# Kernel tuning notes

Hardware: AMD Instinct MI355X
Metric: run time of the kernel (lower is better)

## Reference

```python
import jax, jax.numpy as jnp
import numpy as np

NUM_EXPERTS = 16
TOP_K = 8
INIT_STD = 0.02

def setup_inputs() -> dict:
    key = jax.random.key(0)
    ks = jax.random.split(key, 5)
    B, S, H, I, E = 2, 2048, 2048, 768, NUM_EXPERTS
    return {
        "hidden_states": jax.random.normal(ks[0], (B, S, H), jnp.float32),
        "w_router": jax.random.normal(ks[1], (H, E), jnp.float32) * INIT_STD,
        "w_gate": jax.random.normal(ks[2], (E, H, I), jnp.float32) * INIT_STD,
        "w_up": jax.random.normal(ks[3], (E, H, I), jnp.float32) * INIT_STD,
        "w_down": jax.random.normal(ks[4], (E, I, H), jnp.float32) * INIT_STD,
    }

def reference(hidden_states, w_router, w_gate, w_up, w_down):
    # Router: logits -> fp32 softmax -> top-k -> renormalize (norm_topk_prob=True)
    router_logits = jnp.einsum("bsh,he->bse", hidden_states, w_router)  # [B,S,E]
    routing_weights = jax.nn.softmax(router_logits.astype(jnp.float32), axis=-1)
    topk_w, topk_idx = jax.lax.top_k(routing_weights, k=TOP_K)  # [B,S,K]
    topk_w = topk_w / topk_w.sum(axis=-1, keepdims=True)
    # Dense per-expert combine weights [B,S,E] (sum over top-k slots matching each expert)
    dense_w = jnp.sum(jax.nn.one_hot(topk_idx, NUM_EXPERTS, dtype=topk_w.dtype) * topk_w[..., None], axis=2)
    dense_w = dense_w.astype(hidden_states.dtype)
    # Every expert runs on all tokens (as in the source loop), vectorized over E
    gate = jax.nn.silu(jnp.einsum("bsh,ehi->besi", hidden_states, w_gate))  # [B,E,S,I]
    up = jnp.einsum("bsh,ehi->besi", hidden_states, w_up)
    expert_out = jnp.einsum("besi,eih->besh", gate * up, w_down)  # [B,E,S,H]
    final = jnp.einsum("bse,besh->bsh", dense_w, expert_out)
    return final, router_logits
```

## Files before the change

### kernel.cpp

```cpp
#include <hip/hip_runtime.h>
#include <hip/hip_bf16.h>


typedef __attribute__((ext_vector_type(8))) short short8;
typedef __attribute__((ext_vector_type(4))) float f32x4;

#define NUM_T 4096
#define DH    2048
#define DI    768
#define NE    16
#define DKD   (NE*DI)
#define MAXMT 20
#define FINAL_ELEMS ((size_t)NUM_T*DH)


static __device__ __forceinline__ unsigned short f2bf(float f) {
  unsigned int u = __builtin_bit_cast(unsigned int, f);
  u += 0x7fffu + ((u >> 16) & 1u);
  return (unsigned short)(u >> 16);
}

static __device__ __forceinline__ float bf2f(unsigned short b) {
  unsigned int u = ((unsigned int)b) << 16;
  return __builtin_bit_cast(float, u);
}

static __device__ __forceinline__ void gload16(const void* g, void* l) {
  __builtin_amdgcn_global_load_lds(
      (__attribute__((address_space(1))) void*)(g),
      (__attribute__((address_space(3))) void*)(l), 16, 0, 0);
}


__global__ __launch_bounds__(256)
void cvt_hidden_k(const float* __restrict__ in, unsigned short* __restrict__ out) {
  size_t i = (size_t)blockIdx.x * 256 + threadIdx.x;
  const float4* p = (const float4*)in + i * 2;
  float4 a = p[0], b = p[1];
  short8 v;
  v[0] = (short)f2bf(a.x); v[1] = (short)f2bf(a.y);
  v[2] = (short)f2bf(a.z); v[3] = (short)f2bf(a.w);
  v[4] = (short)f2bf(b.x); v[5] = (short)f2bf(b.y);
  v[6] = (short)f2bf(b.z); v[7] = (short)f2bf(b.w);
  *(short8*)(out + i * 8) = v;
}


__global__ __launch_bounds__(256)
void transpose_cvt_k(const float* __restrict__ in, unsigned short* __restrict__ out,
                     int R, int C, long inStrideE, long outStrideE, int outLD) {
  __shared__ float tile[32][33];
  const float* inE = in + (size_t)blockIdx.z * inStrideE;
  unsigned short* outE = out + (size_t)blockIdx.z * outStrideE;
  int c0 = blockIdx.x * 32, r0 = blockIdx.y * 32;
  int tx = threadIdx.x, ty = threadIdx.y;
#pragma unroll
  for (int i = 0; i < 4; i++)
    tile[ty * 4 + i][tx] = inE[(size_t)(r0 + ty * 4 + i) * C + c0 + tx];
  __syncthreads();
#pragma unroll
  for (int i = 0; i < 4; i++) {
    int c = ty * 4 + i;
    outE[(size_t)(c0 + c) * outLD + r0 + tx] = f2bf(tile[tx][c]);
  }
}


__global__ __launch_bounds__(256)
void router_k(const float* __restrict__ x, const float* __restrict__ wr,
              float* __restrict__ logits_out, unsigned short* __restrict__ dwb) {
  int t = blockIdx.x;
  int tid = threadIdx.x, lane = tid & 63, wid = tid >> 6;
  float acc[16];
#pragma unroll
  for (int e = 0; e < 16; e++) acc[e] = 0.f;
  const float* xt = x + (size_t)t * DH;
  for (int i = tid; i < DH; i += 256) {
    float hv = xt[i];
    const float4* w4 = (const float4*)(wr + (size_t)i * 16);
#pragma unroll
    for (int q = 0; q < 4; q++) {
      float4 w = w4[q];
      acc[q * 4 + 0] += hv * w.x; acc[q * 4 + 1] += hv * w.y;
      acc[q * 4 + 2] += hv * w.z; acc[q * 4 + 3] += hv * w.w;
    }
  }
#pragma unroll
  for (int e = 0; e < 16; e++) {
#pragma unroll
    for (int off = 32; off; off >>= 1) acc[e] += __shfl_xor(acc[e], off, 64);
  }
  __shared__ float red[4][16];
  if (lane == 0) {
#pragma unroll
    for (int e = 0; e < 16; e++) red[wid][e] = acc[e];
  }
  __syncthreads();
  if (tid == 0) {
    float lg[16];
#pragma unroll
    for (int e = 0; e < 16; e++) lg[e] = red[0][e] + red[1][e] + red[2][e] + red[3][e];
    float mx = lg[0];
#pragma unroll
    for (int e = 1; e < 16; e++) mx = fmaxf(mx, lg[e]);
    float p[16], s = 0.f;
#pragma unroll
    for (int e = 0; e < 16; e++) { p[e] = __expf(lg[e] - mx); s += p[e]; }
    float inv = 1.f / s;
#pragma unroll
    for (int e = 0; e < 16; e++) p[e] *= inv;
    float tmp[16];
#pragma unroll
    for (int e = 0; e < 16; e++) tmp[e] = p[e];
    int idx[8]; float val[8]; float ts = 0.f;
#pragma unroll
    for (int k = 0; k < 8; k++) {
      int b = 0; float bv = tmp[0];
#pragma unroll
      for (int e = 1; e < 16; e++) { if (tmp[e] > bv) { bv = tmp[e]; b = e; } }
      idx[k] = b; val[k] = bv; tmp[b] = -1.f; ts += bv;
    }
    float dw[16];
#pragma unroll
    for (int e = 0; e < 16; e++) dw[e] = 0.f;
    float invt = 1.f / ts;
#pragma unroll
    for (int k = 0; k < 8; k++) dw[idx[k]] += val[k] * invt;
#pragma unroll
    for (int e = 0; e < 16; e++) {
      dwb[(size_t)t * 16 + e] = f2bf(dw[e]);
      logits_out[(size_t)t * 16 + e] = lg[e];
    }
  }
}


__global__ __launch_bounds__(256)
void build_lists_k(const unsigned short* __restrict__ dwb,
                   unsigned short* __restrict__ lst) {
  int e = blockIdx.x;
  int tid = threadIdx.x;
  unsigned short loc[16]; int c = 0;
#pragma unroll
  for (int j = 0; j < 16; j++) {
    int t = tid * 16 + j;
    if (dwb[(size_t)t * 16 + e] != 0) loc[c++] = (unsigned short)t;
  }
  __shared__ int sc[256];
  __shared__ int pre[257];
  sc[tid] = c;
  __syncthreads();
  if (tid == 0) {
    int s = 0;
    for (int i = 0; i < 256; i++) { pre[i] = s; s += sc[i]; }
    pre[256] = s;
  }
  __syncthreads();
  unsigned short* L = lst + (size_t)e * NUM_T;
  int base = pre[tid];
  for (int j = 0; j < c; j++) L[base + j] = loc[j];
  int total = pre[256];
  for (int i = total + tid; i < NUM_T; i += 256) L[i] = 0xFFFFu;
}


__global__ __launch_bounds__(256)
void zfill_k(short8* __restrict__ p) {
  size_t i = (size_t)blockIdx.x * 256 + threadIdx.x;
  short8 z = {0,0,0,0,0,0,0,0};
  p[i] = z;
}


__global__ __launch_bounds__(256, 3)
void gateup_k(const unsigned short* __restrict__ hbf,
              const unsigned short* __restrict__ wgbt,
              const unsigned short* __restrict__ wubt,
              const unsigned short* __restrict__ dwb,
              const unsigned short* __restrict__ lst,
              unsigned short* __restrict__ hs) {
  const int bxr = blockIdx.x;
  const int wl  = (bxr & 7) * 480 + (bxr >> 3);
  const int e   = wl / 240;
  const int rem = wl - e * 240;
  const int n0  = (rem / MAXMT) * 64;
  const int m0  = (rem % MAXMT) * 128;

  const unsigned short* L = lst + (size_t)e * NUM_T;
  if (L[m0] == 0xFFFFu) return;

  const int tid = threadIdx.x, lane = tid & 63, wid = tid >> 6;
  const int wm = wid >> 1, wn = wid & 1;
  const int lr = lane & 15, lgp = lane >> 4;

  __shared__ alignas(16) unsigned short As [3 * 128 * 32];
  __shared__ alignas(16) unsigned short Bgs[3 *  64 * 32];
  __shared__ alignas(16) unsigned short Bus[3 *  64 * 32];

  f32x4 zero = {0.f, 0.f, 0.f, 0.f};
  f32x4 accg[4][2], accu[4][2];
#pragma unroll
  for (int m = 0; m < 4; m++)
#pragma unroll
    for (int n = 0; n < 2; n++) { accg[m][n] = zero; accu[m][n] = zero; }

  const unsigned short* wgE = wgbt + (size_t)e * DI * DH;
  const unsigned short* wuE = wubt + (size_t)e * DI * DH;

  const int srow    = lane >> 2;
  const int schunk8 = (((lane & 3) - ((lane >> 3) & 3)) & 3) * 8;

  const int ar0 = m0 + wid * 32 + srow, ar1 = ar0 + 16;
  const unsigned short t0 = L[ar0], t1 = L[ar1];
  const size_t prow0 = (t0 == 0xFFFFu) ? 0 : (size_t)t0;
  const size_t prow1 = (t1 == 0xFFFFu) ? 0 : (size_t)t1;
  const size_t brow = (size_t)(n0 + wid * 16 + srow);

  const int slot8 = (((lane >> 4) + ((lane >> 1) & 3)) & 3) * 8;

  auto stage = [&](int b, int k0) {
    unsigned short* Ab = As  + b * 4096 + wid * 1024;
    unsigned short* Gb = Bgs + b * 2048 + wid * 512;
    unsigned short* Ub = Bus + b * 2048 + wid * 512;
    gload16(hbf + prow0 * DH + k0 + schunk8, Ab);
    gload16(hbf + prow1 * DH + k0 + schunk8, Ab + 512);
    gload16(wgE + brow  * DH + k0 + schunk8, Gb);
    gload16(wuE + brow  * DH + k0 + schunk8, Ub);
  };

  auto compute = [&](int b) {
    const unsigned short* Ab = As  + b * 4096;
    const unsigned short* Gb = Bgs + b * 2048;
    const unsigned short* Ub = Bus + b * 2048;
    short8 a[4], bg[2], bu[2];
#pragma unroll
    for (int m = 0; m < 4; m++)
      a[m] = *(const short8*)(Ab + (wm * 64 + m * 16 + lr) * 32 + slot8);
#pragma unroll
    for (int n = 0; n < 2; n++) {
      bg[n] = *(const short8*)(Gb + (wn * 32 + n * 16 + lr) * 32 + slot8);
      bu[n] = *(const short8*)(Ub + (wn * 32 + n * 16 + lr) * 32 + slot8);
    }
#pragma unroll
    for (int m = 0; m < 4; m++)
#pragma unroll
      for (int n = 0; n < 2; n++) {
        accg[m][n] = __builtin_amdgcn_mfma_f32_16x16x32_bf16(a[m], bg[n], accg[m][n], 0, 0, 0);
        accu[m][n] = __builtin_amdgcn_mfma_f32_16x16x32_bf16(a[m], bu[n], accu[m][n], 0, 0, 0);
      }
  };

  const int NT = DH / 32;
  stage(0, 0);
  stage(1, 32);
  int bc = 0, bs = 2;
#pragma unroll 1
  for (int i = 0; i < NT - 1; ++i) {
    asm volatile("s_waitcnt vmcnt(4)" ::: "memory");
    __builtin_amdgcn_s_barrier();
    __builtin_amdgcn_sched_barrier(0);
    compute(bc);
    if (i + 2 < NT) stage(bs, (i + 2) * 32);
    bc = (bc == 2) ? 0 : bc + 1;
    bs = (bs == 2) ? 0 : bs + 1;
  }
  asm volatile("s_waitcnt vmcnt(0)" ::: "memory");
  __builtin_amdgcn_s_barrier();
  __builtin_amdgcn_sched_barrier(0);
  compute(bc);

#pragma unroll
  for (int m = 0; m < 4; m++) {
#pragma unroll
    for (int r = 0; r < 4; r++) {
      int mrow = m0 + wm * 64 + m * 16 + 4 * lgp + r;
      unsigned short tp = L[mrow];
      if (tp == 0xFFFFu) continue;
      float w = bf2f(dwb[(size_t)tp * 16 + e]);
#pragma unroll
      for (int n = 0; n < 2; n++) {
        float g = accg[m][n][r], u = accu[m][n][r];
        float sig = 1.f / (1.f + __expf(-g));
        float val = g * sig * u * w;
        hs[(size_t)tp * DKD + e * DI + n0 + wn * 32 + n * 16 + lr] = f2bf(val);
      }
    }
  }
}


__global__ __launch_bounds__(256, 3)
void down_k(const unsigned short* __restrict__ hsb,
            const unsigned short* __restrict__ wdbt,
            float* __restrict__ outp) {
  const int bxr = blockIdx.x;
  const int w   = (bxr & 7) * 64 + (bxr >> 3);
  const int m0  = (w & 31) << 7;
  const int n0  = (w >> 5) << 7;

  const int tid = threadIdx.x, lane = tid & 63, wid = tid >> 6;
  const int wm = wid >> 1, wn = wid & 1;
  const int lr = lane & 15, lgp = lane >> 4;

  __shared__ alignas(16) unsigned short As[3 * 128 * 32];
  __shared__ alignas(16) unsigned short Bs[3 * 128 * 32];

  f32x4 zero = {0.f, 0.f, 0.f, 0.f};
  f32x4 acc[4][4];
#pragma unroll
  for (int m = 0; m < 4; m++)
#pragma unroll
    for (int n = 0; n < 4; n++) acc[m][n] = zero;

  const int srow    = lane >> 2;
  const int schunk8 = (((lane & 3) - ((lane >> 3) & 3)) & 3) * 8;
  const int sOff0   = wid * 1024;
  const int sOff1   = sOff0 + 512;
  const size_t arow0 = (size_t)(m0 + wid * 32 + srow), arow1 = arow0 + 16;
  const size_t brow0 = (size_t)(n0 + wid * 32 + srow), brow1 = brow0 + 16;
  const int slot8 = (((lane >> 4) + ((lane >> 1) & 3)) & 3) * 8;

  auto stage = [&](int b, int k0) {
    unsigned short* Ab = As + b * 4096;
    unsigned short* Bb = Bs + b * 4096;
    gload16(hsb  + arow0 * DKD + k0 + schunk8, Ab + sOff0);
    gload16(hsb  + arow1 * DKD + k0 + schunk8, Ab + sOff1);
    gload16(wdbt + brow0 * DKD + k0 + schunk8, Bb + sOff0);
    gload16(wdbt + brow1 * DKD + k0 + schunk8, Bb + sOff1);
  };

  auto compute = [&](int bsel) {
    const unsigned short* Ab = As + bsel * 4096;
    const unsigned short* Bb = Bs + bsel * 4096;
    short8 a[4], b[4];
#pragma unroll
    for (int m = 0; m < 4; m++)
      a[m] = *(const short8*)(Ab + (size_t)(wm * 64 + m * 16 + lr) * 32 + slot8);
#pragma unroll
    for (int n = 0; n < 4; n++)
      b[n] = *(const short8*)(Bb + (size_t)(wn * 64 + n * 16 + lr) * 32 + slot8);
#pragma unroll
    for (int m = 0; m < 4; m++)
#pragma unroll
      for (int n = 0; n < 4; n++)
        acc[m][n] = __builtin_amdgcn_mfma_f32_16x16x32_bf16(a[m], b[n], acc[m][n], 0, 0, 0);
  };

  const int NT = DKD / 32;
  stage(0, 0);
  stage(1, 32);
  int bc = 0, bs = 2;
#pragma unroll 1
  for (int i = 0; i < NT - 1; ++i) {
    asm volatile("s_waitcnt vmcnt(4)" ::: "memory");
    __builtin_amdgcn_s_barrier();
    __builtin_amdgcn_sched_barrier(0);
    compute(bc);
    if (i + 2 < NT) stage(bs, (i + 2) * 32);
    bc = (bc == 2) ? 0 : bc + 1;
    bs = (bs == 2) ? 0 : bs + 1;
  }
  asm volatile("s_waitcnt vmcnt(0)" ::: "memory");
  __builtin_amdgcn_s_barrier();
  __builtin_amdgcn_sched_barrier(0);
  compute(bc);

#pragma unroll
  for (int m = 0; m < 4; m++)
#pragma unroll
    for (int r = 0; r < 4; r++) {
      int t = m0 + wm * 64 + m * 16 + 4 * lgp + r;
#pragma unroll
      for (int n = 0; n < 4; n++)
        outp[(size_t)t * DH + n0 + wn * 64 + n * 16 + lr] = acc[m][n][r];
    }
}


extern "C" void kernel_launch(void* const* d_in, const int* in_sizes, int n_in,
                              void* d_out, int out_size, void* d_ws, size_t ws_size,
                              hipStream_t stream) {
  const float* x  = (const float*)d_in[0];
  const float* wr = (const float*)d_in[1];
  const float* wg = (const float*)d_in[2];
  const float* wu = (const float*)d_in[3];
  const float* wd = (const float*)d_in[4];

  float* outF = (float*)d_out;
  float* outL = outF + FINAL_ELEMS;

  if (ws_size < 218365952ull) return;
  char* ws = (char*)d_ws;
  unsigned short* hbf  = (unsigned short*)(ws);
  unsigned short* wgbt = (unsigned short*)(ws + 16777216);
  unsigned short* wubt = (unsigned short*)(ws + 67108864);
  unsigned short* hs   = (unsigned short*)(ws + 117440512);
  unsigned short* dwb  = (unsigned short*)(ws + 218103808);
  unsigned short* lst  = (unsigned short*)(ws + 218234880);
  unsigned short* wdbt = wgbt;

  cvt_hidden_k<<<4096, 256, 0, stream>>>(x, hbf);
  transpose_cvt_k<<<dim3(24, 64, 16), dim3(32, 8), 0, stream>>>(
      wg, wgbt, 2048, 768, (long)2048 * 768, (long)768 * 2048, 2048);
  transpose_cvt_k<<<dim3(24, 64, 16), dim3(32, 8), 0, stream>>>(
      wu, wubt, 2048, 768, (long)2048 * 768, (long)768 * 2048, 2048);
  router_k<<<4096, 256, 0, stream>>>(x, wr, outL, dwb);
  build_lists_k<<<16, 256, 0, stream>>>(dwb, lst);
  zfill_k<<<24576, 256, 0, stream>>>((short8*)hs);
  gateup_k<<<3840, 256, 0, stream>>>(hbf, wgbt, wubt, dwb, lst, hs);
  transpose_cvt_k<<<dim3(64, 24, 16), dim3(32, 8), 0, stream>>>(
      wd, wdbt, 768, 2048, (long)768 * 2048, 768L, 12288);
  down_k<<<512, 256, 0, stream>>>(hs, wdbt, outF);
}
```

Baseline: 729.0 us.

## Compact per-expert activations and run grouped down projection with slot reduction

The gate/up output is now stored compacted per expert, so only routed token rows exist, instead of as a dense token-by-(expert*I) matrix that needed zero-filling. The down projection becomes a grouped GEMM per expert over only those routed rows, with K=768 instead of 12288. It writes bf16 partial outputs into per-top-k-slot buffers, which a separate kernel sums into the final fp32 output. The work is split into two token halves to fit the workspace. This removes the zero fill and the dense down GEMM's wasted FLOPs, at the cost of extra bf16 partial traffic, a reduction pass, and bf16 rounding of the partials before summation.

```diff
diff --git a/kernel.cpp b/kernel.cpp
--- a/kernel.cpp
+++ b/kernel.cpp
@@ -11,6 +11,8 @@
 #define NE    16
 #define DKD   (NE*DI)
 #define MAXMT 20
+#define HSC_CAP 2560
+#define TOK_HALF 2048
 #define FINAL_ELEMS ((size_t)NUM_T*DH)
 
 
@@ -68,7 +70,8 @@
 
 __global__ __launch_bounds__(256)
 void router_k(const float* __restrict__ x, const float* __restrict__ wr,
-              float* __restrict__ logits_out, unsigned short* __restrict__ dwb) {
+              float* __restrict__ logits_out, unsigned short* __restrict__ dwb,
+              unsigned char* __restrict__ slt) {
   int t = blockIdx.x;
   int tid = threadIdx.x, lane = tid & 63, wid = tid >> 6;
   float acc[16];
@@ -121,14 +124,16 @@
       idx[k] = b; val[k] = bv; tmp[b] = -1.f; ts += bv;
     }
     float dw[16];
-#pragma unroll
-    for (int e = 0; e < 16; e++) dw[e] = 0.f;
+    unsigned char sl[16];
+#pragma unroll
+    for (int e = 0; e < 16; e++) { dw[e] = 0.f; sl[e] = 0xFF; }
     float invt = 1.f / ts;
 #pragma unroll
-    for (int k = 0; k < 8; k++) dw[idx[k]] += val[k] * invt;
+    for (int k = 0; k < 8; k++) { dw[idx[k]] += val[k] * invt; sl[idx[k]] = (unsigned char)k; }
 #pragma unroll
     for (int e = 0; e < 16; e++) {
       dwb[(size_t)t * 16 + e] = f2bf(dw[e]);
+      slt[(size_t)t * 16 + e] = sl[e];
       logits_out[(size_t)t * 16 + e] = lg[e];
     }
   }
@@ -137,14 +142,18 @@
 
 __global__ __launch_bounds__(256)
 void build_lists_k(const unsigned short* __restrict__ dwb,
-                   unsigned short* __restrict__ lst) {
+                   const unsigned char* __restrict__ slt,
+                   unsigned short* __restrict__ lst, int* __restrict__ meta) {
   int e = blockIdx.x;
   int tid = threadIdx.x;
   unsigned short loc[16]; int c = 0;
 #pragma unroll
   for (int j = 0; j < 16; j++) {
     int t = tid * 16 + j;
-    if (dwb[(size_t)t * 16 + e] != 0) loc[c++] = (unsigned short)t;
+    if (dwb[(size_t)t * 16 + e] != 0) {
+      unsigned short s = slt[(size_t)t * 16 + e];
+      loc[c++] = (unsigned short)(t | (s << 12));
+    }
   }
   __shared__ int sc[256];
   __shared__ int pre[257];
@@ -161,14 +170,7 @@
   for (int j = 0; j < c; j++) L[base + j] = loc[j];
   int total = pre[256];
   for (int i = total + tid; i < NUM_T; i += 256) L[i] = 0xFFFFu;
-}
-
-
-__global__ __launch_bounds__(256)
-void zfill_k(short8* __restrict__ p) {
-  size_t i = (size_t)blockIdx.x * 256 + threadIdx.x;
-  short8 z = {0,0,0,0,0,0,0,0};
-  p[i] = z;
+  if (tid == 0) { meta[e * 2] = pre[128]; meta[e * 2 + 1] = total; }
 }
 
 
@@ -178,7 +180,7 @@
               const unsigned short* __restrict__ wubt,
               const unsigned short* __restrict__ dwb,
               const unsigned short* __restrict__ lst,
-              unsigned short* __restrict__ hs) {
+              unsigned short* __restrict__ hsC) {
   const int bxr = blockIdx.x;
   const int wl  = (bxr & 7) * 480 + (bxr >> 3);
   const int e   = wl / 240;
@@ -187,7 +189,7 @@
   const int m0  = (rem % MAXMT) * 128;
 
   const unsigned short* L = lst + (size_t)e * NUM_T;
-  if (L[m0] == 0xFFFFu) return;
+  if (L[m0] & 0x8000) return;
 
   const int tid = threadIdx.x, lane = tid & 63, wid = tid >> 6;
   const int wm = wid >> 1, wn = wid & 1;
@@ -212,8 +214,8 @@
 
   const int ar0 = m0 + wid * 32 + srow, ar1 = ar0 + 16;
   const unsigned short t0 = L[ar0], t1 = L[ar1];
-  const size_t prow0 = (t0 == 0xFFFFu) ? 0 : (size_t)t0;
-  const size_t prow1 = (t1 == 0xFFFFu) ? 0 : (size_t)t1;
+  const size_t prow0 = (t0 & 0x8000) ? 0 : (size_t)(t0 & 0xFFF);
+  const size_t prow1 = (t1 & 0x8000) ? 0 : (size_t)(t1 & 0xFFF);
   const size_t brow = (size_t)(n0 + wid * 16 + srow);
 
   const int slot8 = (((lane >> 4) + ((lane >> 1) & 3)) & 3) * 8;
@@ -274,15 +276,16 @@
 #pragma unroll
     for (int r = 0; r < 4; r++) {
       int mrow = m0 + wm * 64 + m * 16 + 4 * lgp + r;
-      unsigned short tp = L[mrow];
-      if (tp == 0xFFFFu) continue;
+      unsigned short en = L[mrow];
+      if (en & 0x8000) continue;
+      int tp = en & 0xFFF;
       float w = bf2f(dwb[(size_t)tp * 16 + e]);
 #pragma unroll
       for (int n = 0; n < 2; n++) {
         float g = accg[m][n][r], u = accu[m][n][r];
         float sig = 1.f / (1.f + __expf(-g));
         float val = g * sig * u * w;
-        hs[(size_t)tp * DKD + e * DI + n0 + wn * 32 + n * 16 + lr] = f2bf(val);
+        hsC[((size_t)e * HSC_CAP + mrow) * DI + n0 + wn * 32 + n * 16 + lr] = f2bf(val);
       }
     }
   }
@@ -290,13 +293,22 @@
 
 
 __global__ __launch_bounds__(256, 3)
-void down_k(const unsigned short* __restrict__ hsb,
-            const unsigned short* __restrict__ wdbt,
-            float* __restrict__ outp) {
+void down_half_k(const unsigned short* __restrict__ hsC,
+                 const unsigned short* __restrict__ wdbt,
+                 const unsigned short* __restrict__ lst,
+                 const int* __restrict__ meta,
+                 unsigned short* __restrict__ slotbuf, int hf) {
   const int bxr = blockIdx.x;
-  const int w   = (bxr & 7) * 64 + (bxr >> 3);
-  const int m0  = (w & 31) << 7;
-  const int n0  = (w >> 5) << 7;
+  const int wl  = (bxr & 7) * 320 + (bxr >> 3);
+  const int e   = wl / 160;
+  const int rem = wl - e * 160;
+  const int n0  = (rem / 10) * 128;
+  const int m0  = (rem % 10) * 128;
+
+  const int rs = hf ? meta[e * 2] : 0;
+  const int re = hf ? meta[e * 2 + 1] : meta[e * 2];
+  const int rcount = re - rs;
+  if (m0 >= rcount) return;
 
   const int tid = threadIdx.x, lane = tid & 63, wid = tid >> 6;
   const int wm = wid >> 1, wn = wid & 1;
@@ -316,17 +328,20 @@
   const int schunk8 = (((lane & 3) - ((lane >> 3) & 3)) & 3) * 8;
   const int sOff0   = wid * 1024;
   const int sOff1   = sOff0 + 512;
-  const size_t arow0 = (size_t)(m0 + wid * 32 + srow), arow1 = arow0 + 16;
+  const size_t arow0 = (size_t)(e * HSC_CAP + rs + m0 + wid * 32 + srow);
+  const size_t arow1 = arow0 + 16;
   const size_t brow0 = (size_t)(n0 + wid * 32 + srow), brow1 = brow0 + 16;
   const int slot8 = (((lane >> 4) + ((lane >> 1) & 3)) & 3) * 8;
+
+  const unsigned short* wdE = wdbt + (size_t)e * DI;
 
   auto stage = [&](int b, int k0) {
     unsigned short* Ab = As + b * 4096;
     unsigned short* Bb = Bs + b * 4096;
-    gload16(hsb  + arow0 * DKD + k0 + schunk8, Ab + sOff0);
-    gload16(hsb  + arow1 * DKD + k0 + schunk8, Ab + sOff1);
-    gload16(wdbt + brow0 * DKD + k0 + schunk8, Bb + sOff0);
-    gload16(wdbt + brow1 * DKD + k0 + schunk8, Bb + sOff1);
+    gload16(hsC + arow0 * DI + k0 + schunk8, Ab + sOff0);
+    gload16(hsC + arow1 * DI + k0 + schunk8, Ab + sOff1);
+    gload16(wdE + brow0 * DKD + k0 + schunk8, Bb + sOff0);
+    gload16(wdE + brow1 * DKD + k0 + schunk8, Bb + sOff1);
   };
 
   auto compute = [&](int bsel) {
@@ -346,7 +361,7 @@
         acc[m][n] = __builtin_amdgcn_mfma_f32_16x16x32_bf16(a[m], b[n], acc[m][n], 0, 0, 0);
   };
 
-  const int NT = DKD / 32;
+  const int NT = DI / 32;
   stage(0, 0);
   stage(1, 32);
   int bc = 0, bs = 2;
@@ -365,15 +380,46 @@
   __builtin_amdgcn_sched_barrier(0);
   compute(bc);
 
-#pragma unroll
-  for (int m = 0; m < 4; m++)
+  const unsigned short* L = lst + (size_t)e * NUM_T;
+#pragma unroll
+  for (int m = 0; m < 4; m++) {
 #pragma unroll
     for (int r = 0; r < 4; r++) {
-      int t = m0 + wm * 64 + m * 16 + 4 * lgp + r;
+      int gr = m0 + wm * 64 + m * 16 + 4 * lgp + r;
+      if (gr >= rcount) continue;
+      unsigned short en = L[rs + gr];
+      int t  = en & 0xFFF;
+      int s  = (en >> 12) & 7;
+      int tl = t - hf * TOK_HALF;
 #pragma unroll
       for (int n = 0; n < 4; n++)
-        outp[(size_t)t * DH + n0 + wn * 64 + n * 16 + lr] = acc[m][n][r];
-    }
+        slotbuf[((size_t)s * TOK_HALF + tl) * DH + n0 + wn * 64 + n * 16 + lr] =
+            f2bf(acc[m][n][r]);
+    }
+  }
+}
+
+
+__global__ __launch_bounds__(256)
+void reduce_half_k(const unsigned short* __restrict__ slotbuf,
+                   float* __restrict__ outp, int hf) {
+  size_t i  = (size_t)blockIdx.x * 256 + threadIdx.x;
+  size_t tl = i >> 8;
+  size_t h0 = (i & 255) * 8;
+  float sum[8];
+#pragma unroll
+  for (int j = 0; j < 8; j++) sum[j] = 0.f;
+#pragma unroll
+  for (int s = 0; s < 8; s++) {
+    short8 v = *(const short8*)(slotbuf + ((size_t)s * TOK_HALF + tl) * DH + h0);
+#pragma unroll
+    for (int j = 0; j < 8; j++) sum[j] += bf2f((unsigned short)v[j]);
+  }
+  float* o = outp + ((size_t)(hf * TOK_HALF) + tl) * DH + h0;
+  float4 o0 = {sum[0], sum[1], sum[2], sum[3]};
+  float4 o1 = {sum[4], sum[5], sum[6], sum[7]};
+  *(float4*)o = o0;
+  *(float4*)(o + 4) = o1;
 }
 
 
@@ -389,26 +435,31 @@
   float* outF = (float*)d_out;
   float* outL = outF + FINAL_ELEMS;
 
-  if (ws_size < 218365952ull) return;
+  if (ws_size < 180682880ull) return;
   char* ws = (char*)d_ws;
-  unsigned short* hbf  = (unsigned short*)(ws);
-  unsigned short* wgbt = (unsigned short*)(ws + 16777216);
-  unsigned short* wubt = (unsigned short*)(ws + 67108864);
-  unsigned short* hs   = (unsigned short*)(ws + 117440512);
-  unsigned short* dwb  = (unsigned short*)(ws + 218103808);
-  unsigned short* lst  = (unsigned short*)(ws + 218234880);
-  unsigned short* wdbt = wgbt;
+  unsigned short* hbf   = (unsigned short*)(ws);
+  unsigned short* wubt  = (unsigned short*)(ws + 16777216);
+  unsigned short* hsC   = (unsigned short*)(ws + 67108864);
+  unsigned short* wgbt  = (unsigned short*)(ws + 130023424);
+  unsigned short* dwb   = (unsigned short*)(ws + 180355072);
+  unsigned short* lst   = (unsigned short*)(ws + 180486144);
+  unsigned char*  slt   = (unsigned char*) (ws + 180617216);
+  int*            meta  = (int*)           (ws + 180682752);
+  unsigned short* sbuf  = (unsigned short*)(ws);
+  unsigned short* wdbt  = wgbt;
 
   cvt_hidden_k<<<4096, 256, 0, stream>>>(x, hbf);
   transpose_cvt_k<<<dim3(24, 64, 16), dim3(32, 8), 0, stream>>>(
       wg, wgbt, 2048, 768, (long)2048 * 768, (long)768 * 2048, 2048);
   transpose_cvt_k<<<dim3(24, 64, 16), dim3(32, 8), 0, stream>>>(
       wu, wubt, 2048, 768, (long)2048 * 768, (long)768 * 2048, 2048);
-  router_k<<<4096, 256, 0, stream>>>(x, wr, outL, dwb);
-  build_lists_k<<<16, 256, 0, stream>>>(dwb, lst);
-  zfill_k<<<24576, 256, 0, stream>>>((short8*)hs);
-  gateup_k<<<3840, 256, 0, stream>>>(hbf, wgbt, wubt, dwb, lst, hs);
+  router_k<<<4096, 256, 0, stream>>>(x, wr, outL, dwb, slt);
+  build_lists_k<<<16, 256, 0, stream>>>(dwb, slt, lst, meta);
+  gateup_k<<<3840, 256, 0, stream>>>(hbf, wgbt, wubt, dwb, lst, hsC);
   transpose_cvt_k<<<dim3(64, 24, 16), dim3(32, 8), 0, stream>>>(
       wd, wdbt, 768, 2048, (long)768 * 2048, 768L, 12288);
-  down_k<<<512, 256, 0, stream>>>(hs, wdbt, outF);
-}
+  down_half_k<<<2560, 256, 0, stream>>>(hsC, wdbt, lst, meta, sbuf, 0);
+  reduce_half_k<<<2048, 256, 0, stream>>>(sbuf, outF, 0);
+  down_half_k<<<2560, 256, 0, stream>>>(hsC, wdbt, lst, meta, sbuf, 1);
+  reduce_half_k<<<2048, 256, 0, stream>>>(sbuf, outF, 1);
+}
```

Result: faster. 638.8 us (-12.4%).
